# Optimization experiments

Hardware: AMD Instinct MI355X
Metric: run time of the kernel (lower is better)

## Reference

```python
import jax, jax.numpy as jnp
import numpy as np

TOKEN_SIZE = 16
STRIDE = 8
EMBED_DIM = 512


def setup_inputs() -> dict:
    key = jax.random.key(0)
    k1, k2 = jax.random.split(key)
    B, S, D = 32, 4096, EMBED_DIM
    x = jax.random.normal(k1, (B, S, D), dtype=jnp.float32)
    fan_in = TOKEN_SIZE * D
    W = jax.random.normal(k2, (fan_in, D), dtype=jnp.float32) / np.sqrt(fan_in)
    b = jnp.zeros((D,), dtype=jnp.float32)
    gamma = jnp.ones((D,), dtype=jnp.float32)
    beta = jnp.zeros((D,), dtype=jnp.float32)
    return {"x": x, "W": W, "b": b, "gamma": gamma, "beta": beta}


def reference(x, W, b, gamma, beta):
    B, S, D = x.shape
    n_win = (S - TOKEN_SIZE) // STRIDE + 1
    # gather all sliding windows at once: [n_win, token_size] index matrix
    idx = jnp.arange(n_win)[:, None] * STRIDE + jnp.arange(TOKEN_SIZE)[None, :]
    win = x[:, idx, :]                       # [B, n_win, token_size, D]
    win = win.reshape(B, n_win, TOKEN_SIZE * D)  # flatten each window
    h = jnp.einsum('bnf,fd->bnd', win, W) + b    # batched GEMM
    h = jax.nn.gelu(h, approximate=False)        # torch GELU default = exact erf
    # LayerNorm over last dim (eps matches torch default 1e-5)
    mu = jnp.mean(h, axis=-1, keepdims=True)
    var = jnp.var(h, axis=-1, keepdims=True)
    h = (h - mu) * jax.lax.rsqrt(var + 1e-5)
    return h * gamma + beta                      # [B, n_win, D]
```

## Files before the change

### kernel.cpp

```cpp
#include <hip/hip_runtime.h>
#include <hip/hip_bf16.h>
#include <cstdint>

#define S_LEN 4096
#define D_DIM 512
#define NWIN  511
#define KDIM  8192
#define THREADS 512

typedef __attribute__((ext_vector_type(8))) short short8;
typedef __attribute__((ext_vector_type(4))) float f32x4;

__device__ __forceinline__ unsigned short f2b(float f) {
    union { float f; unsigned int u; } v; v.f = f;
    unsigned int r = v.u + 0x7FFFu + ((v.u >> 16) & 1u);
    return (unsigned short)(r >> 16);
}

__global__ void wpack_kernel(const float* __restrict__ W, short8* __restrict__ pk) {
    __shared__ float tile[64][68];
    const int b2 = blockIdx.x;
    const int s = b2 >> 3, w = b2 & 7;
    const int t = s >> 3, c0 = (s & 7) << 6;
    const int tid = threadIdx.x;
    {
        int r = tid >> 2, c4 = (tid & 3) << 4;
        const float* src = W + (size_t)(t * 512 + c0 + r) * D_DIM + (w << 6) + c4;
#pragma unroll
        for (int j = 0; j < 4; ++j) {
            float4 v = *(const float4*)(src + 4 * j);
            tile[r][c4 + 4 * j + 0] = v.x;
            tile[r][c4 + 4 * j + 1] = v.y;
            tile[r][c4 + 4 * j + 2] = v.z;
            tile[r][c4 + 4 * j + 3] = v.w;
        }
    }
    __syncthreads();
    const int lane = tid & 63, f2 = tid >> 6;
#pragma unroll
    for (int ff = 0; ff < 2; ++ff) {
        int f = f2 * 2 + ff;
        int n = f >> 1, k32 = f & 1;
        short8 u;
#pragma unroll
        for (int e = 0; e < 8; ++e)
            u[e] = (short)f2b(tile[k32 * 32 + (lane >> 4) * 8 + e][n * 16 + (lane & 15)]);
        pk[((size_t)b2 * 8 + f) * 64 + lane] = u;
    }
}

__device__ __forceinline__ void load_b(const short8* __restrict__ pk, int s, int wid,
                                       int lane, short8 (&b)[4][2]) {
    const short8* base = pk + ((size_t)(s * 8 + wid) * 8) * 64 + lane;
#pragma unroll
    for (int n = 0; n < 4; ++n)
#pragma unroll
        for (int k32 = 0; k32 < 2; ++k32)
            b[n][k32] = base[(n * 2 + k32) * 64];
}

__global__ __launch_bounds__(THREADS, 2)
void fused_kernel(const float* __restrict__ x,
                  const short8* __restrict__ pk,
                  const float* __restrict__ bias,
                  const float* __restrict__ gamma,
                  const float* __restrict__ beta,
                  float* __restrict__ out)
{
    __shared__ __align__(16) unsigned short lsA[2][64 * 64];
    __shared__ float redS[8][64];
    __shared__ float redQ[8][64];

    const int blk = blockIdx.x;
    const int b  = blk >> 3;
    const int n0 = (blk & 7) << 6;
    const int tid = threadIdx.x;
    const int lane = tid & 63;
    const int wid  = tid >> 6;
    const int r15 = lane & 15, hi = lane >> 4;
    const int ai = tid >> 3, ak8 = tid & 7;
    const int akb = ak8 ^ (ai & 7);
    const float* xb = x + (size_t)b * S_LEN * D_DIM;

    f32x4 acc[4][4] = {};
    short8 bc[4][2], bn[4][2];

    {
        int row = 8 * (n0 + ai) + 0;
        if (row > S_LEN - 1) row = S_LEN - 1;
        const float* src = xb + (size_t)row * D_DIM + 0 + ak8 * 8;
        float4 f0 = *(const float4*)src;
        float4 f1 = *(const float4*)(src + 4);
        short8 u;
        u[0] = (short)f2b(f0.x); u[1] = (short)f2b(f0.y);
        u[2] = (short)f2b(f0.z); u[3] = (short)f2b(f0.w);
        u[4] = (short)f2b(f1.x); u[5] = (short)f2b(f1.y);
        u[6] = (short)f2b(f1.z); u[7] = (short)f2b(f1.w);
        *(short8*)&lsA[0][ai * 64 + akb * 8] = u;
        load_b(pk, 0, wid, lane, bc);
    }
    __syncthreads();

#define STEP(S, CUR, NXT, BCUR, BNXT)                                          \
    {                                                                          \
        const int sn = ((S) + 1) & 127;                                        \
                                                   \
        load_b(pk, sn, wid, lane, BNXT);                                       \
                    \
        const int tn = sn >> 3, c0n = (sn & 7) << 6;                           \
        int rown = 8 * (n0 + ai) + tn;                                         \
        if (rown > S_LEN - 1) rown = S_LEN - 1;                                \
        const float* asrc = xb + (size_t)rown * D_DIM + c0n + ak8 * 8;         \
        float4 f0 = *(const float4*)asrc;                                      \
        float4 f1 = *(const float4*)(asrc + 4);                                \
                                               \
        short8 afr[4][2];                                                      \
        _Pragma("unroll")                                                      \
        for (int m = 0; m < 4; ++m) {                                          \
            int row = 16 * m + r15;                                            \
            _Pragma("unroll")                                                  \
            for (int k32 = 0; k32 < 2; ++k32) {                                \
                int kb = (k32 * 4 + hi) ^ (row & 7);                           \
                afr[m][k32] = *(const short8*)&lsA[CUR][row * 64 + kb * 8];    \
            }                                                                  \
        }                                                                      \
                                                             \
        _Pragma("unroll")                                                      \
        for (int k32 = 0; k32 < 2; ++k32)                                      \
            _Pragma("unroll")                                                  \
            for (int m = 0; m < 4; ++m)                                        \
                _Pragma("unroll")                                              \
                for (int n = 0; n < 4; ++n)                                    \
                    acc[m][n] = __builtin_amdgcn_mfma_f32_16x16x32_bf16(       \
                        afr[m][k32], BCUR[n][k32], acc[m][n], 0, 0, 0);        \
                                    \
        short8 u;                                                              \
        u[0] = (short)f2b(f0.x); u[1] = (short)f2b(f0.y);                      \
        u[2] = (short)f2b(f0.z); u[3] = (short)f2b(f0.w);                      \
        u[4] = (short)f2b(f1.x); u[5] = (short)f2b(f1.y);                      \
        u[6] = (short)f2b(f1.z); u[7] = (short)f2b(f1.w);                      \
        *(short8*)&lsA[NXT][ai * 64 + akb * 8] = u;                            \
        __syncthreads();                                                       \
    }

    for (int it = 0; it < 64; ++it) {
        STEP(it * 2,     0, 1, bc, bn)
        STEP(it * 2 + 1, 1, 0, bn, bc)
    }
#undef STEP

    float bias4[4], gam4[4], bet4[4];
#pragma unroll
    for (int n = 0; n < 4; ++n) {
        int d = (wid << 6) + 16 * n + r15;
        bias4[n] = bias[d]; gam4[n] = gamma[d]; bet4[n] = beta[d];
    }
    float sum_[4][4], sq_[4][4];
#pragma unroll
    for (int m = 0; m < 4; ++m)
#pragma unroll
        for (int r = 0; r < 4; ++r) { sum_[m][r] = 0.f; sq_[m][r] = 0.f; }
#pragma unroll
    for (int m = 0; m < 4; ++m)
#pragma unroll
        for (int n = 0; n < 4; ++n)
#pragma unroll
            for (int r = 0; r < 4; ++r) {
                float h = acc[m][n][r] + bias4[n];
                float g = 0.5f * h * (1.0f + erff(h * 0.70710678118654752f));
                acc[m][n][r] = g;
                sum_[m][r] += g;
                sq_[m][r]  += g * g;
            }
#pragma unroll
    for (int m = 0; m < 4; ++m)
#pragma unroll
        for (int r = 0; r < 4; ++r) {
            float sv = sum_[m][r], qv = sq_[m][r];
#pragma unroll
            for (int msk = 1; msk < 16; msk <<= 1) {
                sv += __shfl_xor(sv, msk, 64);
                qv += __shfl_xor(qv, msk, 64);
            }
            sum_[m][r] = sv; sq_[m][r] = qv;
        }
    if (r15 == 0) {
#pragma unroll
        for (int m = 0; m < 4; ++m)
#pragma unroll
            for (int r = 0; r < 4; ++r) {
                int row16 = 16 * m + hi * 4 + r;
                redS[wid][row16] = sum_[m][r];
                redQ[wid][row16] = sq_[m][r];
            }
    }
    __syncthreads();
#pragma unroll
    for (int m = 0; m < 4; ++m) {
#pragma unroll
        for (int r = 0; r < 4; ++r) {
            int row16 = 16 * m + hi * 4 + r;
            float sv = 0.f, qv = 0.f;
#pragma unroll
            for (int w = 0; w < 8; ++w) { sv += redS[w][row16]; qv += redQ[w][row16]; }
            float mu  = sv * (1.0f / 512.0f);
            float var = qv * (1.0f / 512.0f) - mu * mu;
            float inv = rsqrtf(var + 1e-5f);
            int win = n0 + row16;
            if (win < NWIN) {
                size_t obase = ((size_t)b * NWIN + win) * D_DIM;
#pragma unroll
                for (int n = 0; n < 4; ++n) {
                    int d = (wid << 6) + 16 * n + r15;
                    out[obase + d] = (acc[m][n][r] - mu) * inv * gam4[n] + bet4[n];
                }
            }
        }
    }
}

__global__ void naive_kernel(const float* __restrict__ x, const float* __restrict__ W,
                             const float* __restrict__ bias, const float* __restrict__ gamma,
                             const float* __restrict__ beta, float* __restrict__ out) {
    __shared__ float hrow[D_DIM];
    __shared__ float red[2];
    const int b = blockIdx.x / NWIN, win = blockIdx.x % NWIN;
    const int d = threadIdx.x;
    float a = 0.f;
    for (int t = 0; t < 16; ++t) {
        const float* xr = x + ((size_t)b * S_LEN + 8 * win + t) * D_DIM;
        const float* wr = W + (size_t)t * D_DIM * D_DIM;
        for (int k = 0; k < D_DIM; ++k) a += xr[k] * wr[(size_t)k * D_DIM + d];
    }
    a += bias[d];
    a = 0.5f * a * (1.0f + erff(a * 0.70710678118654752f));
    hrow[d] = a;
    __syncthreads();
    if (d == 0) {
        float s = 0.f, q = 0.f;
        for (int k = 0; k < D_DIM; ++k) { s += hrow[k]; q += hrow[k] * hrow[k]; }
        float mu = s / D_DIM;
        red[0] = mu; red[1] = rsqrtf(q / D_DIM - mu * mu + 1e-5f);
    }
    __syncthreads();
    out[((size_t)b * NWIN + win) * D_DIM + d] = (a - red[0]) * red[1] * gamma[d] + beta[d];
}

extern "C" void kernel_launch(void* const* d_in, const int* in_sizes, int n_in,
                              void* d_out, int out_size, void* d_ws, size_t ws_size,
                              hipStream_t stream) {
    const float* x     = (const float*)d_in[0];
    const float* W     = (const float*)d_in[1];
    const float* bias  = (const float*)d_in[2];
    const float* gamma = (const float*)d_in[3];
    const float* beta  = (const float*)d_in[4];
    float* out = (float*)d_out;

    const size_t pk_bytes = (size_t)KDIM * D_DIM * sizeof(unsigned short);
    if (ws_size >= pk_bytes) {
        short8* pk = (short8*)d_ws;
        wpack_kernel<<<1024, 256, 0, stream>>>(W, (short8*)pk);
        fused_kernel<<<256, THREADS, 0, stream>>>(x, pk, bias, gamma, beta, out);
    } else {
        naive_kernel<<<32 * NWIN, D_DIM, 0, stream>>>(x, W, bias, gamma, beta, out);
    }
}
```

Measured before the change: 218.3 us.

## Stage contiguous input row slab in LDS and reuse across window offsets

Reorders the K loop so that each 64-column chunk of a contiguous 520-row slab of x is loaded once into LDS and reused across all 16 token offsets. Previously each of the 128 K-steps loaded a fresh strided 64x64 tile with a barrier per step. The weight packing is reordered to match the new K ordering. Global loads for the next chunk are spread across the token steps to overlap with the MFMAs, and barriers drop to one per chunk. The cost is a much larger LDS footprint (about 133 KB for the double buffer) and many more live registers for prefetch, which may limit occupancy to one block per CU.

```diff
diff --git a/kernel.cpp b/kernel.cpp
--- a/kernel.cpp
+++ b/kernel.cpp
@@ -6,7 +6,8 @@
 #define D_DIM 512
 #define NWIN  511
 #define KDIM  8192
-#define THREADS 512
+#define TROWS 520
+#define ASLOTS (TROWS * 8)
 
 typedef __attribute__((ext_vector_type(8))) short short8;
 typedef __attribute__((ext_vector_type(4))) float f32x4;
@@ -21,11 +22,12 @@
     __shared__ float tile[64][68];
     const int b2 = blockIdx.x;
     const int s = b2 >> 3, w = b2 & 7;
-    const int t = s >> 3, c0 = (s & 7) << 6;
+    const int t = s >> 3, c0 = s & 7;
+    const int q = c0 * 16 + t;
     const int tid = threadIdx.x;
     {
         int r = tid >> 2, c4 = (tid & 3) << 4;
-        const float* src = W + (size_t)(t * 512 + c0 + r) * D_DIM + (w << 6) + c4;
+        const float* src = W + (size_t)(t * 512 + c0 * 64 + r) * D_DIM + (w << 6) + c4;
 #pragma unroll
         for (int j = 0; j < 4; ++j) {
             float4 v = *(const float4*)(src + 4 * j);
@@ -45,21 +47,21 @@
 #pragma unroll
         for (int e = 0; e < 8; ++e)
             u[e] = (short)f2b(tile[k32 * 32 + (lane >> 4) * 8 + e][n * 16 + (lane & 15)]);
-        pk[((size_t)b2 * 8 + f) * 64 + lane] = u;
-    }
-}
-
-__device__ __forceinline__ void load_b(const short8* __restrict__ pk, int s, int wid,
-                                       int lane, short8 (&b)[4][2]) {
-    const short8* base = pk + ((size_t)(s * 8 + wid) * 8) * 64 + lane;
+        pk[((size_t)q * 8 + w) * 8 * 64 + (size_t)f * 64 + lane] = u;
+    }
+}
+
+__device__ __forceinline__ void load_b(const short8* __restrict__ pk, int q, int wslot,
+                                       int lane, short8 (&bf)[4][2]) {
+    const short8* base = pk + ((size_t)(q * 8 + wslot) * 8) * 64 + lane;
 #pragma unroll
     for (int n = 0; n < 4; ++n)
 #pragma unroll
         for (int k32 = 0; k32 < 2; ++k32)
-            b[n][k32] = base[(n * 2 + k32) * 64];
-}
-
-__global__ __launch_bounds__(THREADS, 2)
+            bf[n][k32] = base[(n * 2 + k32) * 64];
+}
+
+__global__ __launch_bounds__(512, 2)
 void fused_kernel(const float* __restrict__ x,
                   const short8* __restrict__ pk,
                   const float* __restrict__ bias,
@@ -67,7 +69,7 @@
                   const float* __restrict__ beta,
                   float* __restrict__ out)
 {
-    __shared__ __align__(16) unsigned short lsA[2][64 * 64];
+    __shared__ __align__(16) unsigned short lsA[2][TROWS * 64];
     __shared__ float redS[8][64];
     __shared__ float redQ[8][64];
 
@@ -78,53 +80,53 @@
     const int lane = tid & 63;
     const int wid  = tid >> 6;
     const int r15 = lane & 15, hi = lane >> 4;
-    const int ai = tid >> 3, ak8 = tid & 7;
-    const int akb = ak8 ^ (ai & 7);
     const float* xb = x + (size_t)b * S_LEN * D_DIM;
 
     f32x4 acc[4][4] = {};
     short8 bc[4][2], bn[4][2];
-
-    {
-        int row = 8 * (n0 + ai) + 0;
-        if (row > S_LEN - 1) row = S_LEN - 1;
-        const float* src = xb + (size_t)row * D_DIM + 0 + ak8 * 8;
-        float4 f0 = *(const float4*)src;
-        float4 f1 = *(const float4*)(src + 4);
-        short8 u;
-        u[0] = (short)f2b(f0.x); u[1] = (short)f2b(f0.y);
-        u[2] = (short)f2b(f0.z); u[3] = (short)f2b(f0.w);
-        u[4] = (short)f2b(f1.x); u[5] = (short)f2b(f1.y);
-        u[6] = (short)f2b(f1.z); u[7] = (short)f2b(f1.w);
-        *(short8*)&lsA[0][ai * 64 + akb * 8] = u;
-        load_b(pk, 0, wid, lane, bc);
-    }
-    __syncthreads();
-
-#define STEP(S, CUR, NXT, BCUR, BNXT)                                          \
+    float4 ta[9][2];
+
+#define CISSUE(J, C0N)                                                         \
     {                                                                          \
-        const int sn = ((S) + 1) & 127;                                        \
-                                                   \
-        load_b(pk, sn, wid, lane, BNXT);                                       \
-                    \
-        const int tn = sn >> 3, c0n = (sn & 7) << 6;                           \
-        int rown = 8 * (n0 + ai) + tn;                                         \
-        if (rown > S_LEN - 1) rown = S_LEN - 1;                                \
-        const float* asrc = xb + (size_t)rown * D_DIM + c0n + ak8 * 8;         \
-        float4 f0 = *(const float4*)asrc;                                      \
-        float4 f1 = *(const float4*)(asrc + 4);                                \
-                                               \
+        if ((J) < 8 || tid < 64) {                                             \
+            const int slot = tid + ((J) << 9);                                 \
+            const int r = slot >> 3, k8 = slot & 7;                            \
+            int grow = 8 * n0 + r;                                             \
+            if (grow > S_LEN - 1) grow = S_LEN - 1;                            \
+            const float* src = xb + (size_t)grow * D_DIM + ((C0N) << 6) + (k8 << 3); \
+            ta[J][0] = *(const float4*)src;                                    \
+            ta[J][1] = *(const float4*)(src + 4);                              \
+        }                                                                      \
+    }
+
+#define CWRITE(J, DST)                                                         \
+    {                                                                          \
+        if ((J) < 8 || tid < 64) {                                             \
+            const int slot = tid + ((J) << 9);                                 \
+            const int r = slot >> 3, k8 = slot & 7;                            \
+            short8 u;                                                          \
+            u[0] = (short)f2b(ta[J][0].x); u[1] = (short)f2b(ta[J][0].y);      \
+            u[2] = (short)f2b(ta[J][0].z); u[3] = (short)f2b(ta[J][0].w);      \
+            u[4] = (short)f2b(ta[J][1].x); u[5] = (short)f2b(ta[J][1].y);      \
+            u[6] = (short)f2b(ta[J][1].z); u[7] = (short)f2b(ta[J][1].w);      \
+            *(short8*)&(DST)[(r << 6) + ((k8 ^ ((r >> 3) & 7)) << 3)] = u;     \
+        }                                                                      \
+    }
+
+#define TSTEP(T, LA, BCUR, BNXT)                                               \
+    {                                                                          \
+        const int qn = (c0 * 16 + (T) + 1) & 127;                              \
+        load_b(pk, qn, wid, lane, BNXT);                                       \
         short8 afr[4][2];                                                      \
         _Pragma("unroll")                                                      \
         for (int m = 0; m < 4; ++m) {                                          \
-            int row = 16 * m + r15;                                            \
+            const int row = (((m << 4) + r15) << 3) + (T);                     \
+            const int sb  = (r15 + ((T) >> 3)) & 7;                            \
             _Pragma("unroll")                                                  \
-            for (int k32 = 0; k32 < 2; ++k32) {                                \
-                int kb = (k32 * 4 + hi) ^ (row & 7);                           \
-                afr[m][k32] = *(const short8*)&lsA[CUR][row * 64 + kb * 8];    \
-            }                                                                  \
+            for (int k32 = 0; k32 < 2; ++k32)                                  \
+                afr[m][k32] = *(const short8*)&(LA)[(row << 6) +               \
+                                   ((((k32 << 2) + hi) ^ sb) << 3)];           \
         }                                                                      \
-                                                             \
         _Pragma("unroll")                                                      \
         for (int k32 = 0; k32 < 2; ++k32)                                      \
             _Pragma("unroll")                                                  \
@@ -133,21 +135,56 @@
                 for (int n = 0; n < 4; ++n)                                    \
                     acc[m][n] = __builtin_amdgcn_mfma_f32_16x16x32_bf16(       \
                         afr[m][k32], BCUR[n][k32], acc[m][n], 0, 0, 0);        \
-                                    \
-        short8 u;                                                              \
-        u[0] = (short)f2b(f0.x); u[1] = (short)f2b(f0.y);                      \
-        u[2] = (short)f2b(f0.z); u[3] = (short)f2b(f0.w);                      \
-        u[4] = (short)f2b(f1.x); u[5] = (short)f2b(f1.y);                      \
-        u[6] = (short)f2b(f1.z); u[7] = (short)f2b(f1.w);                      \
-        *(short8*)&lsA[NXT][ai * 64 + akb * 8] = u;                            \
-        __syncthreads();                                                       \
-    }
-
-    for (int it = 0; it < 64; ++it) {
-        STEP(it * 2,     0, 1, bc, bn)
-        STEP(it * 2 + 1, 1, 0, bn, bc)
-    }
-#undef STEP
+    }
+
+    load_b(pk, 0, wid, lane, bc);
+    CISSUE(0, 0) CISSUE(1, 0) CISSUE(2, 0) CISSUE(3, 0) CISSUE(4, 0)
+    CISSUE(5, 0) CISSUE(6, 0) CISSUE(7, 0) CISSUE(8, 0)
+    CWRITE(0, lsA[0]) CWRITE(1, lsA[0]) CWRITE(2, lsA[0]) CWRITE(3, lsA[0])
+    CWRITE(4, lsA[0]) CWRITE(5, lsA[0]) CWRITE(6, lsA[0]) CWRITE(7, lsA[0])
+    CWRITE(8, lsA[0])
+    asm volatile("s_waitcnt lgkmcnt(0)" ::: "memory");
+    __builtin_amdgcn_s_barrier();
+    __builtin_amdgcn_sched_barrier(0);
+
+    for (int c0 = 0; c0 < 8; ++c0) {
+        const unsigned short* La = lsA[c0 & 1];
+        unsigned short* Ln = lsA[(c0 + 1) & 1];
+        const int c0n = c0 + 1;
+        const int pf = (c0 < 7);
+
+        TSTEP(0, La, bc, bn)
+        if (pf) { CISSUE(0, c0n) CISSUE(1, c0n) }
+        TSTEP(1, La, bn, bc)
+        TSTEP(2, La, bc, bn)
+        if (pf) { CISSUE(2, c0n) CISSUE(3, c0n) }
+        TSTEP(3, La, bn, bc)
+        TSTEP(4, La, bc, bn)
+        if (pf) { CISSUE(4, c0n) CISSUE(5, c0n) }
+        TSTEP(5, La, bn, bc)
+        TSTEP(6, La, bc, bn)
+        if (pf) { CISSUE(6, c0n) CISSUE(7, c0n) }
+        TSTEP(7, La, bn, bc)
+        TSTEP(8, La, bc, bn)
+        if (pf) { CISSUE(8, c0n) CWRITE(0, Ln) CWRITE(1, Ln) }
+        TSTEP(9, La, bn, bc)
+        TSTEP(10, La, bc, bn)
+        if (pf) { CWRITE(2, Ln) CWRITE(3, Ln) }
+        TSTEP(11, La, bn, bc)
+        TSTEP(12, La, bc, bn)
+        if (pf) { CWRITE(4, Ln) CWRITE(5, Ln) }
+        TSTEP(13, La, bn, bc)
+        TSTEP(14, La, bc, bn)
+        if (pf) { CWRITE(6, Ln) CWRITE(7, Ln) CWRITE(8, Ln) }
+        TSTEP(15, La, bn, bc)
+
+        asm volatile("s_waitcnt lgkmcnt(0)" ::: "memory");
+        __builtin_amdgcn_s_barrier();
+        __builtin_amdgcn_sched_barrier(0);
+    }
+#undef TSTEP
+#undef CISSUE
+#undef CWRITE
 
     float bias4[4], gam4[4], bet4[4];
 #pragma unroll
@@ -259,8 +296,8 @@
     const size_t pk_bytes = (size_t)KDIM * D_DIM * sizeof(unsigned short);
     if (ws_size >= pk_bytes) {
         short8* pk = (short8*)d_ws;
-        wpack_kernel<<<1024, 256, 0, stream>>>(W, (short8*)pk);
-        fused_kernel<<<256, THREADS, 0, stream>>>(x, pk, bias, gamma, beta, out);
+        wpack_kernel<<<1024, 256, 0, stream>>>(W, pk);
+        fused_kernel<<<256, 512, 0, stream>>>(x, pk, bias, gamma, beta, out);
     } else {
         naive_kernel<<<32 * NWIN, D_DIM, 0, stream>>>(x, W, bias, gamma, beta, out);
     }
```

Result: faster. 176.5 us (-19.1%).

## Exploit window overlap by staging raw rows once and splitting LayerNorm out

Applied to the files above, without the earlier changes.

Restructures the GEMM so each block loads a contiguous span of x rows into LDS once per 32-column slice. Every window then reads its 16 tokens from that shared buffer instead of re-gathering overlapping windows, which removes the 2x redundant x traffic and conversion. Each block now covers 128 windows by 256 output columns with 16 waves, and uses a new packed-W layout ordered by column slice and token. Because a block no longer sees full rows, GELU output is written to a workspace buffer and a separate LayerNorm kernel normalizes it. That adds an extra round trip of the intermediate through global memory plus one more launch.

```diff
diff --git a/kernel.cpp b/kernel.cpp
--- a/kernel.cpp
+++ b/kernel.cpp
@@ -6,9 +6,10 @@
 #define D_DIM 512
 #define NWIN  511
 #define KDIM  8192
-#define THREADS 512
+#define TR2   1032
 
 typedef __attribute__((ext_vector_type(8))) short short8;
+typedef __attribute__((ext_vector_type(4))) short short4v;
 typedef __attribute__((ext_vector_type(4))) float f32x4;
 
 __device__ __forceinline__ unsigned short f2b(float f) {
@@ -17,15 +18,15 @@
     return (unsigned short)(r >> 16);
 }
 
-__global__ void wpack_kernel(const float* __restrict__ W, short8* __restrict__ pk) {
+__global__ void wpack2_kernel(const float* __restrict__ W, short8* __restrict__ pk) {
     __shared__ float tile[64][68];
     const int b2 = blockIdx.x;
     const int s = b2 >> 3, w = b2 & 7;
-    const int t = s >> 3, c0 = (s & 7) << 6;
+    const int t = s >> 3, c0 = s & 7;
     const int tid = threadIdx.x;
     {
         int r = tid >> 2, c4 = (tid & 3) << 4;
-        const float* src = W + (size_t)(t * 512 + c0 + r) * D_DIM + (w << 6) + c4;
+        const float* src = W + (size_t)(t * 512 + c0 * 64 + r) * D_DIM + (w << 6) + c4;
 #pragma unroll
         for (int j = 0; j < 4; ++j) {
             float4 v = *(const float4*)(src + 4 * j);
@@ -37,185 +38,194 @@
     }
     __syncthreads();
     const int lane = tid & 63, f2 = tid >> 6;
+    const int r15 = lane & 15, hi = lane >> 4;
 #pragma unroll
     for (int ff = 0; ff < 2; ++ff) {
         int f = f2 * 2 + ff;
         int n = f >> 1, k32 = f & 1;
+        int q2 = (c0 * 2 + k32) * 16 + t;
         short8 u;
 #pragma unroll
         for (int e = 0; e < 8; ++e)
-            u[e] = (short)f2b(tile[k32 * 32 + (lane >> 4) * 8 + e][n * 16 + (lane & 15)]);
-        pk[((size_t)b2 * 8 + f) * 64 + lane] = u;
-    }
-}
-
-__device__ __forceinline__ void load_b(const short8* __restrict__ pk, int s, int wid,
-                                       int lane, short8 (&b)[4][2]) {
-    const short8* base = pk + ((size_t)(s * 8 + wid) * 8) * 64 + lane;
-#pragma unroll
-    for (int n = 0; n < 4; ++n)
-#pragma unroll
-        for (int k32 = 0; k32 < 2; ++k32)
-            b[n][k32] = base[(n * 2 + k32) * 64];
-}
-
-__global__ __launch_bounds__(THREADS, 2)
-void fused_kernel(const float* __restrict__ x,
+            u[e] = (short)f2b(tile[k32 * 32 + hi * 8 + e][n * 16 + r15]);
+        pk[(size_t)q2 * 2048 + w * 256 + n * 64 + lane] = u;
+    }
+}
+
+__global__ __launch_bounds__(1024)
+void gemm2_kernel(const float* __restrict__ x,
                   const short8* __restrict__ pk,
                   const float* __restrict__ bias,
-                  const float* __restrict__ gamma,
-                  const float* __restrict__ beta,
-                  float* __restrict__ out)
+                  float* __restrict__ hbuf)
 {
-    __shared__ __align__(16) unsigned short lsA[2][64 * 64];
-    __shared__ float redS[8][64];
-    __shared__ float redQ[8][64];
-
-    const int blk = blockIdx.x;
-    const int b  = blk >> 3;
-    const int n0 = (blk & 7) << 6;
-    const int tid = threadIdx.x;
-    const int lane = tid & 63;
-    const int wid  = tid >> 6;
+    __shared__ __align__(16) unsigned short lsA[2][TR2 * 32];
+
+    const int p  = blockIdx.x;
+    const int nc = (p >> 3) & 1;
+    const int g  = ((p >> 4) << 3) | (p & 7);
+    const int b  = g >> 2;
+    const int n0 = (g & 3) << 7;
+    const int tid  = threadIdx.x;
+    const int lane = tid & 63, wid = tid >> 6;
     const int r15 = lane & 15, hi = lane >> 4;
-    const int ai = tid >> 3, ak8 = tid & 7;
-    const int akb = ak8 ^ (ai & 7);
+    const int boff = (nc * 4 + (wid >> 2)) * 256 + (wid & 3) * 64 + lane;
     const float* xb = x + (size_t)b * S_LEN * D_DIM;
 
-    f32x4 acc[4][4] = {};
-    short8 bc[4][2], bn[4][2];
-
-    {
-        int row = 8 * (n0 + ai) + 0;
-        if (row > S_LEN - 1) row = S_LEN - 1;
-        const float* src = xb + (size_t)row * D_DIM + 0 + ak8 * 8;
-        float4 f0 = *(const float4*)src;
-        float4 f1 = *(const float4*)(src + 4);
-        short8 u;
-        u[0] = (short)f2b(f0.x); u[1] = (short)f2b(f0.y);
-        u[2] = (short)f2b(f0.z); u[3] = (short)f2b(f0.w);
-        u[4] = (short)f2b(f1.x); u[5] = (short)f2b(f1.y);
-        u[6] = (short)f2b(f1.z); u[7] = (short)f2b(f1.w);
-        *(short8*)&lsA[0][ai * 64 + akb * 8] = u;
-        load_b(pk, 0, wid, lane, bc);
-    }
-    __syncthreads();
-
-#define STEP(S, CUR, NXT, BCUR, BNXT)                                          \
+    f32x4 acc[8] = {};
+    short8 B0, B1, B2, B3;
+    float4 ta[2][2];
+
+#define CISSUE(J, SL)                                                          \
     {                                                                          \
-        const int sn = ((S) + 1) & 127;                                        \
-                                                   \
-        load_b(pk, sn, wid, lane, BNXT);                                       \
-                    \
-        const int tn = sn >> 3, c0n = (sn & 7) << 6;                           \
-        int rown = 8 * (n0 + ai) + tn;                                         \
-        if (rown > S_LEN - 1) rown = S_LEN - 1;                                \
-        const float* asrc = xb + (size_t)rown * D_DIM + c0n + ak8 * 8;         \
-        float4 f0 = *(const float4*)asrc;                                      \
-        float4 f1 = *(const float4*)(asrc + 4);                                \
-                                               \
-        short8 afr[4][2];                                                      \
+        if ((J) < 4 || tid < 32) {                                             \
+            const int c_ = tid + ((J) << 10);                                  \
+            const int r_ = c_ >> 2, kc_ = c_ & 3;                              \
+            int gr_ = 8 * n0 + r_;                                             \
+            if (gr_ > S_LEN - 1) gr_ = S_LEN - 1;                              \
+            const float* s_ = xb + (size_t)gr_ * D_DIM + (SL) * 32 + (kc_ << 3); \
+            ta[(J) & 1][0] = *(const float4*)s_;                               \
+            ta[(J) & 1][1] = *(const float4*)(s_ + 4);                         \
+        }                                                                      \
+    }
+
+#define CWRITE(J, DST)                                                         \
+    {                                                                          \
+        if ((J) < 4 || tid < 32) {                                             \
+            const int c_ = tid + ((J) << 10);                                  \
+            const int r_ = c_ >> 2, kc_ = c_ & 3;                              \
+            const int sw_ = (r_ >> 3) & 7;                                     \
+            short4v lo_, hh_;                                                  \
+            lo_[0] = (short)f2b(ta[(J) & 1][0].x);                             \
+            lo_[1] = (short)f2b(ta[(J) & 1][0].y);                             \
+            lo_[2] = (short)f2b(ta[(J) & 1][0].z);                             \
+            lo_[3] = (short)f2b(ta[(J) & 1][0].w);                             \
+            hh_[0] = (short)f2b(ta[(J) & 1][1].x);                             \
+            hh_[1] = (short)f2b(ta[(J) & 1][1].y);                             \
+            hh_[2] = (short)f2b(ta[(J) & 1][1].z);                             \
+            hh_[3] = (short)f2b(ta[(J) & 1][1].w);                             \
+            *(short4v*)&(DST)[r_ * 32 + ((((kc_ << 1)    ) ^ sw_) << 2)] = lo_; \
+            *(short4v*)&(DST)[r_ * 32 + ((((kc_ << 1) | 1) ^ sw_) << 2)] = hh_; \
+        }                                                                      \
+    }
+
+#define TSTEP(T, LA, BU, BL)                                                   \
+    {                                                                          \
+        BL = pk[(size_t)((u0 + (T) + 2) & 255) * 2048 + boff];                 \
+        const int swr = (r15 + ((T) >> 3)) & 7;                                \
         _Pragma("unroll")                                                      \
-        for (int m = 0; m < 4; ++m) {                                          \
-            int row = 16 * m + r15;                                            \
-            _Pragma("unroll")                                                  \
-            for (int k32 = 0; k32 < 2; ++k32) {                                \
-                int kb = (k32 * 4 + hi) ^ (row & 7);                           \
-                afr[m][k32] = *(const short8*)&lsA[CUR][row * 64 + kb * 8];    \
-            }                                                                  \
+        for (int m = 0; m < 8; ++m) {                                          \
+            const int rb = (8 * ((m << 4) + r15) + (T)) * 32;                  \
+            short4v alo = *(const short4v*)&(LA)[rb + ((( (hi << 1)     ) ^ swr) << 2)]; \
+            short4v ahi = *(const short4v*)&(LA)[rb + ((( (hi << 1) | 1 ) ^ swr) << 2)]; \
+            short8 afr = __builtin_shufflevector(alo, ahi, 0, 1, 2, 3, 4, 5, 6, 7);      \
+            acc[m] = __builtin_amdgcn_mfma_f32_16x16x32_bf16(afr, BU, acc[m], 0, 0, 0);  \
         }                                                                      \
-                                                             \
-        _Pragma("unroll")                                                      \
-        for (int k32 = 0; k32 < 2; ++k32)                                      \
-            _Pragma("unroll")                                                  \
-            for (int m = 0; m < 4; ++m)                                        \
-                _Pragma("unroll")                                              \
-                for (int n = 0; n < 4; ++n)                                    \
-                    acc[m][n] = __builtin_amdgcn_mfma_f32_16x16x32_bf16(       \
-                        afr[m][k32], BCUR[n][k32], acc[m][n], 0, 0, 0);        \
-                                    \
-        short8 u;                                                              \
-        u[0] = (short)f2b(f0.x); u[1] = (short)f2b(f0.y);                      \
-        u[2] = (short)f2b(f0.z); u[3] = (short)f2b(f0.w);                      \
-        u[4] = (short)f2b(f1.x); u[5] = (short)f2b(f1.y);                      \
-        u[6] = (short)f2b(f1.z); u[7] = (short)f2b(f1.w);                      \
-        *(short8*)&lsA[NXT][ai * 64 + akb * 8] = u;                            \
-        __syncthreads();                                                       \
-    }
-
-    for (int it = 0; it < 64; ++it) {
-        STEP(it * 2,     0, 1, bc, bn)
-        STEP(it * 2 + 1, 1, 0, bn, bc)
-    }
-#undef STEP
-
-    float bias4[4], gam4[4], bet4[4];
-#pragma unroll
-    for (int n = 0; n < 4; ++n) {
-        int d = (wid << 6) + 16 * n + r15;
-        bias4[n] = bias[d]; gam4[n] = gamma[d]; bet4[n] = beta[d];
-    }
-    float sum_[4][4], sq_[4][4];
-#pragma unroll
-    for (int m = 0; m < 4; ++m)
-#pragma unroll
-        for (int r = 0; r < 4; ++r) { sum_[m][r] = 0.f; sq_[m][r] = 0.f; }
-#pragma unroll
-    for (int m = 0; m < 4; ++m)
-#pragma unroll
-        for (int n = 0; n < 4; ++n)
-#pragma unroll
-            for (int r = 0; r < 4; ++r) {
-                float h = acc[m][n][r] + bias4[n];
-                float g = 0.5f * h * (1.0f + erff(h * 0.70710678118654752f));
-                acc[m][n][r] = g;
-                sum_[m][r] += g;
-                sq_[m][r]  += g * g;
-            }
-#pragma unroll
-    for (int m = 0; m < 4; ++m)
+    }
+
+    B0 = pk[(size_t)0 * 2048 + boff];
+    B1 = pk[(size_t)1 * 2048 + boff];
+    CISSUE(0, 0) CISSUE(1, 0) CWRITE(0, lsA[0]) CISSUE(2, 0) CWRITE(1, lsA[0])
+    CISSUE(3, 0) CWRITE(2, lsA[0]) CISSUE(4, 0) CWRITE(3, lsA[0]) CWRITE(4, lsA[0])
+    asm volatile("s_waitcnt lgkmcnt(0)" ::: "memory");
+    __builtin_amdgcn_s_barrier();
+    __builtin_amdgcn_sched_barrier(0);
+
+    for (int sl = 0; sl < 16; ++sl) {
+        const unsigned short* La = lsA[sl & 1];
+        unsigned short* Ln = lsA[(sl + 1) & 1];
+        const int u0 = sl << 4;
+        const int snx = sl + 1;
+        const int pf = (sl < 15);
+
+        TSTEP(0, La, B0, B2)
+        if (pf) CISSUE(0, snx)
+        TSTEP(1, La, B1, B3)
+        if (pf) CISSUE(1, snx)
+        TSTEP(2, La, B2, B0)
+        TSTEP(3, La, B3, B1)
+        if (pf) { CWRITE(0, Ln) CISSUE(2, snx) }
+        TSTEP(4, La, B0, B2)
+        TSTEP(5, La, B1, B3)
+        if (pf) { CWRITE(1, Ln) CISSUE(3, snx) }
+        TSTEP(6, La, B2, B0)
+        TSTEP(7, La, B3, B1)
+        if (pf) { CWRITE(2, Ln) CISSUE(4, snx) }
+        TSTEP(8, La, B0, B2)
+        TSTEP(9, La, B1, B3)
+        if (pf) CWRITE(3, Ln)
+        TSTEP(10, La, B2, B0)
+        TSTEP(11, La, B3, B1)
+        if (pf) CWRITE(4, Ln)
+        TSTEP(12, La, B0, B2)
+        TSTEP(13, La, B1, B3)
+        TSTEP(14, La, B2, B0)
+        TSTEP(15, La, B3, B1)
+
+        asm volatile("s_waitcnt lgkmcnt(0)" ::: "memory");
+        __builtin_amdgcn_s_barrier();
+        __builtin_amdgcn_sched_barrier(0);
+    }
+#undef TSTEP
+#undef CISSUE
+#undef CWRITE
+
+    const int d = nc * 256 + (wid << 4) + r15;
+    const float bias1 = bias[d];
+    float* hb = hbuf + (size_t)b * NWIN * D_DIM;
+#pragma unroll
+    for (int m = 0; m < 8; ++m) {
 #pragma unroll
         for (int r = 0; r < 4; ++r) {
-            float sv = sum_[m][r], qv = sq_[m][r];
-#pragma unroll
-            for (int msk = 1; msk < 16; msk <<= 1) {
-                sv += __shfl_xor(sv, msk, 64);
-                qv += __shfl_xor(qv, msk, 64);
-            }
-            sum_[m][r] = sv; sq_[m][r] = qv;
-        }
-    if (r15 == 0) {
-#pragma unroll
-        for (int m = 0; m < 4; ++m)
-#pragma unroll
-            for (int r = 0; r < 4; ++r) {
-                int row16 = 16 * m + hi * 4 + r;
-                redS[wid][row16] = sum_[m][r];
-                redQ[wid][row16] = sq_[m][r];
-            }
-    }
-    __syncthreads();
-#pragma unroll
-    for (int m = 0; m < 4; ++m) {
-#pragma unroll
-        for (int r = 0; r < 4; ++r) {
-            int row16 = 16 * m + hi * 4 + r;
-            float sv = 0.f, qv = 0.f;
-#pragma unroll
-            for (int w = 0; w < 8; ++w) { sv += redS[w][row16]; qv += redQ[w][row16]; }
-            float mu  = sv * (1.0f / 512.0f);
-            float var = qv * (1.0f / 512.0f) - mu * mu;
-            float inv = rsqrtf(var + 1e-5f);
-            int win = n0 + row16;
+            int win = n0 + (m << 4) + (hi << 2) + r;
             if (win < NWIN) {
-                size_t obase = ((size_t)b * NWIN + win) * D_DIM;
-#pragma unroll
-                for (int n = 0; n < 4; ++n) {
-                    int d = (wid << 6) + 16 * n + r15;
-                    out[obase + d] = (acc[m][n][r] - mu) * inv * gam4[n] + bet4[n];
-                }
+                float h = acc[m][r] + bias1;
+                hb[(size_t)win * D_DIM + d] =
+                    0.5f * h * (1.0f + erff(h * 0.70710678118654752f));
             }
         }
+    }
+}
+
+__global__ __launch_bounds__(256, 8)
+void ln_kernel(const float* __restrict__ h, const float* __restrict__ gamma,
+               const float* __restrict__ beta, float* __restrict__ out, int nrows)
+{
+    const int lane = threadIdx.x & 63;
+    const int wv = blockIdx.x * 4 + (threadIdx.x >> 6);
+    const int nw = gridDim.x * 4;
+    float gm[8], bt[8];
+#pragma unroll
+    for (int j = 0; j < 8; ++j) {
+        gm[j] = gamma[lane * 8 + j];
+        bt[j] = beta[lane * 8 + j];
+    }
+    for (int row = wv; row < nrows; row += nw) {
+        const float* src = h + (size_t)row * D_DIM + lane * 8;
+        float4 v0 = *(const float4*)src;
+        float4 v1 = *(const float4*)(src + 4);
+        float s = v0.x + v0.y + v0.z + v0.w + v1.x + v1.y + v1.z + v1.w;
+        float q = v0.x * v0.x + v0.y * v0.y + v0.z * v0.z + v0.w * v0.w +
+                  v1.x * v1.x + v1.y * v1.y + v1.z * v1.z + v1.w * v1.w;
+#pragma unroll
+        for (int msk = 1; msk < 64; msk <<= 1) {
+            s += __shfl_xor(s, msk, 64);
+            q += __shfl_xor(q, msk, 64);
+        }
+        float mu  = s * (1.0f / 512.0f);
+        float inv = rsqrtf(q * (1.0f / 512.0f) - mu * mu + 1e-5f);
+        float o[8] = { v0.x, v0.y, v0.z, v0.w, v1.x, v1.y, v1.z, v1.w };
+        float4 r0, r1;
+        r0.x = (o[0] - mu) * inv * gm[0] + bt[0];
+        r0.y = (o[1] - mu) * inv * gm[1] + bt[1];
+        r0.z = (o[2] - mu) * inv * gm[2] + bt[2];
+        r0.w = (o[3] - mu) * inv * gm[3] + bt[3];
+        r1.x = (o[4] - mu) * inv * gm[4] + bt[4];
+        r1.y = (o[5] - mu) * inv * gm[5] + bt[5];
+        r1.z = (o[6] - mu) * inv * gm[6] + bt[6];
+        r1.w = (o[7] - mu) * inv * gm[7] + bt[7];
+        float* dst = out + (size_t)row * D_DIM + lane * 8;
+        *(float4*)dst = r0;
+        *(float4*)(dst + 4) = r1;
     }
 }
 
@@ -257,10 +267,14 @@
     float* out = (float*)d_out;
 
     const size_t pk_bytes = (size_t)KDIM * D_DIM * sizeof(unsigned short);
-    if (ws_size >= pk_bytes) {
+    const size_t h_bytes  = (size_t)32 * NWIN * D_DIM * sizeof(float);
+
+    if (ws_size >= pk_bytes + h_bytes) {
         short8* pk = (short8*)d_ws;
-        wpack_kernel<<<1024, 256, 0, stream>>>(W, (short8*)pk);
-        fused_kernel<<<256, THREADS, 0, stream>>>(x, pk, bias, gamma, beta, out);
+        float* hbuf = (float*)((char*)d_ws + pk_bytes);
+        wpack2_kernel<<<1024, 256, 0, stream>>>(W, pk);
+        gemm2_kernel<<<256, 1024, 0, stream>>>(x, pk, bias, hbuf);
+        ln_kernel<<<1024, 256, 0, stream>>>(hbuf, gamma, beta, out, 32 * NWIN);
     } else {
         naive_kernel<<<32 * NWIN, D_DIM, 0, stream>>>(x, W, bias, gamma, beta, out);
     }
```

Result: slower. 339.6 us (+55.6%).
